# Kernel optimization log

Measured on AMD Instinct MI355X. Metric: run time of the kernel, lower is better.

## Reference

```python
import jax, jax.numpy as jnp
import numpy as np

N_HEAD = 16

def setup_inputs() -> dict:
    key = jax.random.key(0)
    ks = jax.random.split(key, 5)
    B, T, C = 2, 2048, 1024
    s = 1.0 / np.sqrt(C)
    return {
        "x":  jax.random.normal(ks[0], (B, T, C), jnp.float32),
        "Wk": jax.random.normal(ks[1], (C, C), jnp.float32) * s,
        "Wq": jax.random.normal(ks[2], (C, C), jnp.float32) * s,
        "Wv": jax.random.normal(ks[3], (C, C), jnp.float32) * s,
        "Wp": jax.random.normal(ks[4], (C, C), jnp.float32) * s,
    }

def reference(x, Wk, Wq, Wv, Wp):
    B, T, C = x.shape
    H = N_HEAD
    D = C // H
    # torch Linear (bias=False): y = x @ W.T
    def proj(W):
        return (x @ W.T).reshape(B, T, H, D).transpose(0, 2, 1, 3)  # [B,H,T,D]
    q, k, v = proj(Wq), proj(Wk), proj(Wv)
    att = jnp.einsum("bhtd,bhsd->bhts", q, k) / jnp.sqrt(jnp.float32(D))
    causal = jnp.tril(jnp.ones((T, T), dtype=bool))
    att = jnp.where(causal[None, None], att, -jnp.inf)
    att = jax.nn.softmax(att, axis=-1)
    y = jnp.einsum("bhts,bhsd->bhtd", att, v)
    y = y.transpose(0, 2, 1, 3).reshape(B, T, C)
    return y @ Wp.T
```

## Files before the change

kernel.cpp:

```cpp
#include <hip/hip_runtime.h>

typedef unsigned short u16;
typedef unsigned int u32;
typedef unsigned long long u64;
typedef __attribute__((ext_vector_type(8))) short bf16x8;
typedef __attribute__((ext_vector_type(8))) _Float16 f16x8;
typedef __attribute__((ext_vector_type(2))) _Float16 f16x2;
typedef __attribute__((ext_vector_type(4))) float f32x4;

#define GLOAD16(gp, lp) __builtin_amdgcn_global_load_lds( \
  (const __attribute__((address_space(1))) unsigned int*)(gp), \
  (__attribute__((address_space(3))) unsigned int*)(lp), 16, 0, 0)

__device__ __forceinline__ u16 f2bf(float f) {
  unsigned int u = __builtin_bit_cast(unsigned int, f);
  u += 0x7fffu + ((u >> 16) & 1u);
  return (u16)(u >> 16);
}

__device__ __forceinline__ u32 pk2(float a, float b) {
  return (u32)f2bf(a) | ((u32)f2bf(b) << 16);
}

__device__ __forceinline__ u32 pkh(float a, float b) {
  return __builtin_bit_cast(u32, __builtin_amdgcn_cvt_pkrtz(a, b));
}

__device__ __forceinline__ void wait_barrier() {
  asm volatile("s_waitcnt vmcnt(0)" ::: "memory");
  __builtin_amdgcn_s_barrier();
  __builtin_amdgcn_sched_barrier(0);
}

__global__ __launch_bounds__(256) void cvt_f32_bf16(
    const float* __restrict__ in, u16* __restrict__ out, int n) {
  int i = (blockIdx.x * 256 + threadIdx.x) * 4;
  if (i < n) {
    float4 f = *reinterpret_cast<const float4*>(in + i);
    u64 v = (u64)pk2(f.x, f.y) | ((u64)pk2(f.z, f.w) << 32);
    *reinterpret_cast<u64*>(out + i) = v;
  }
}

__global__ __launch_bounds__(256) void cvt_w4(
    const float* __restrict__ w0, const float* __restrict__ w1,
    const float* __restrict__ w2, const float* __restrict__ w3,
    u16* __restrict__ o0, u16* __restrict__ o1,
    u16* __restrict__ o2, u16* __restrict__ o3) {
  int z = blockIdx.y;
  const float* in = (z == 0) ? w0 : (z == 1) ? w1 : (z == 2) ? w2 : w3;
  u16* out = (z == 0) ? o0 : (z == 1) ? o1 : (z == 2) ? o2 : o3;
  int i = (blockIdx.x * 256 + threadIdx.x) * 4;
  float4 f = *reinterpret_cast<const float4*>(in + i);
  u64 v = (u64)pk2(f.x, f.y) | ((u64)pk2(f.z, f.w) << 32);
  *reinterpret_cast<u64*>(out + i) = v;
}

template<int MODE, int MI>
__device__ __forceinline__ void gemm_bt_body(
    const u16* __restrict__ A, const u16* __restrict__ Bw, void* __restrict__ Cout,
    int m0, int n0, float scale) {
  const int K = 1024;
  __shared__ __align__(16) u16 As[2][MI * 32 * 32];
  __shared__ __align__(16) u16 Bs[2][128 * 32];
  const int tid = threadIdx.x;
  const int lane = tid & 63, wid = tid >> 6;
  const int wr = wid >> 1, wc = wid & 1;
  const int g = lane >> 4, c = lane & 15;
  f32x4 acc[MI][4] = {};

  auto stage = [&](int buf, int k0) {
#pragma unroll
    for (int i = 0; i < MI / 2; ++i) {
      int idx = tid + i * 256;
      int row = idx >> 2, slot = idx & 3;
      int ss = slot ^ (row & 3);
      GLOAD16(A + (size_t)(m0 + row) * K + k0 + ss * 8, &As[buf][idx * 8]);
    }
#pragma unroll
    for (int i = 0; i < 2; ++i) {
      int idx = tid + i * 256;
      int row = idx >> 2, slot = idx & 3;
      int ss = slot ^ (row & 3);
      GLOAD16(Bw + (size_t)(n0 + row) * K + k0 + ss * 8, &Bs[buf][idx * 8]);
    }
  };

  stage(0, 0);
  int buf = 0;
#pragma unroll 1
  for (int kt = 0; kt < 32; ++kt) {
    wait_barrier();
    if (kt + 1 < 32) stage(buf ^ 1, (kt + 1) * 32);
    bf16x8 af[MI], bfr[4];
#pragma unroll
    for (int mi = 0; mi < MI; ++mi) {
      int row = wr * (MI * 16) + mi * 16 + c;
      int slot = g ^ (row & 3);
      af[mi] = *(const bf16x8*)&As[buf][row * 32 + slot * 8];
    }
#pragma unroll
    for (int ni = 0; ni < 4; ++ni) {
      int row = wc * 64 + ni * 16 + c;
      int slot = g ^ (row & 3);
      bfr[ni] = *(const bf16x8*)&Bs[buf][row * 32 + slot * 8];
    }
    __builtin_amdgcn_s_setprio(1);
#pragma unroll
    for (int mi = 0; mi < MI; ++mi)
#pragma unroll
      for (int ni = 0; ni < 4; ++ni)
        acc[mi][ni] = __builtin_amdgcn_mfma_f32_16x16x32_bf16(af[mi], bfr[ni], acc[mi][ni], 0, 0, 0);
    __builtin_amdgcn_s_setprio(0);
    buf ^= 1;
  }

#pragma unroll
  for (int mi = 0; mi < MI; ++mi)
#pragma unroll
    for (int ni = 0; ni < 4; ++ni)
#pragma unroll
      for (int i = 0; i < 4; ++i) {
        int m = m0 + wr * (MI * 16) + mi * 16 + g * 4 + i;
        int n = n0 + wc * 64 + ni * 16 + c;
        float v = acc[mi][ni][i];
        if (MODE == 0) {
          int b = m >> 11, t = m & 2047, h = n >> 6, d = n & 63;
          ((u16*)Cout)[(((size_t)b * 16 + h) * 2048 + t) * 64 + d] = f2bf(v * scale);
        } else {
          ((float*)Cout)[(size_t)m * 1024 + n] = v;
        }
      }
}

#define QSCALE 0.1803368801111204f

__global__ __launch_bounds__(256, 3) void proj_qkv(
    const u16* __restrict__ xb, const u16* __restrict__ wq, const u16* __restrict__ wk,
    const u16* __restrict__ wv, u16* __restrict__ q, u16* __restrict__ k, u16* __restrict__ v) {
  int z = blockIdx.z;
  const u16* W = (z == 0) ? wq : (z == 1) ? wk : wv;
  u16* O = (z == 0) ? q : (z == 1) ? k : v;
  float scale = (z == 0) ? QSCALE : 1.0f;
  gemm_bt_body<0, 4>(xb, W, O, blockIdx.y * 128, blockIdx.x * 128, scale);
}

__global__ __launch_bounds__(256, 2) void gemm_out(
    const u16* __restrict__ y, const u16* __restrict__ wp, float* __restrict__ out) {
  gemm_bt_body<1, 2>(y, wp, out, blockIdx.y * 64, blockIdx.x * 128, 1.0f);
}

__global__ __launch_bounds__(256) void transpose_v_kernel(
    const u16* __restrict__ v, u16* __restrict__ vt) {
  __shared__ u16 tile[64][65];
  int bh = blockIdx.y, t0 = blockIdx.x * 64;
  const u16* src = v + ((size_t)bh * 2048 + t0) * 64;
  u16* dst = vt + (size_t)bh * 64 * 2048 + t0;
  int tid = threadIdx.x;
#pragma unroll
  for (int i = 0; i < 16; ++i) {
    int idx = tid + i * 256;
    tile[idx >> 6][idx & 63] = src[idx];
  }
  __syncthreads();
#pragma unroll
  for (int i = 0; i < 16; ++i) {
    int idx = tid + i * 256;
    int d = idx >> 6, j = idx & 63;
    int t = ((j & 3) << 4) | (j >> 2);
    float f = __builtin_bit_cast(float, (u32)tile[t][d] << 16);
    _Float16 hh = (_Float16)f;
    dst[(size_t)d * 2048 + j] = __builtin_bit_cast(u16, hh);
  }
}

__global__ __launch_bounds__(256, 4) void attn_kernel(
    const u16* __restrict__ q, const u16* __restrict__ kg,
    const u16* __restrict__ vt, u16* __restrict__ y) {
  const int T = 2048;
  __shared__ __align__(16) u16 Ks[2][64 * 64];
  __shared__ __align__(16) u16 Vs[2][64 * 64];
  __shared__ __align__(16) u16 Ps[4][16 * 64];
  const int tid = threadIdx.x, lane = tid & 63, w = tid >> 6;
  const int g = lane >> 4, c = lane & 15;
  const int bh = blockIdx.x;
  const int qt = 31 - (int)blockIdx.y;
  const u16* Q = q + (size_t)bh * T * 64;
  const u16* K = kg + (size_t)bh * T * 64;
  const u16* V = vt + (size_t)bh * 64 * T;
  const int b = bh >> 4, h = bh & 15;
  const int qrow0 = qt * 64 + w * 16;

  f16x8 ones;
#pragma unroll
  for (int j = 0; j < 8; ++j) ones[j] = (_Float16)1.0f;

  auto stage = [&](int bb, int j0) {
#pragma unroll
    for (int i = 0; i < 2; ++i) {
      int idx = tid + i * 256;
      int row = idx >> 3, slot = idx & 7;
      int ss = slot ^ (row & 7);
      GLOAD16(K + (size_t)(j0 + row) * 64 + ss * 8, &Ks[bb][idx * 8]);
      GLOAD16(V + (size_t)row * T + j0 + ss * 8, &Vs[bb][idx * 8]);
    }
  };

  bf16x8 qf[2];
#pragma unroll
  for (int kk = 0; kk < 2; ++kk)
    qf[kk] = *(const bf16x8*)&Q[(size_t)(qrow0 + c) * 64 + kk * 32 + g * 8];

  f32x4 o[4] = {};
  f32x4 ol = {};

  const int nkt = qt + 1;
  stage(0, 0);
  int buf = 0;
#pragma unroll 1
  for (int kt = 0; kt < nkt; ++kt) {
    const int j0 = kt * 64;
    wait_barrier();
    if (kt + 1 < nkt) stage(buf ^ 1, j0 + 64);

    bf16x8 kb[4][2];
#pragma unroll
    for (int ni = 0; ni < 4; ++ni)
#pragma unroll
      for (int kk = 0; kk < 2; ++kk) {
        int kr = ni * 16 + c;
        int slot = (kk * 4 + g) ^ (kr & 7);
        kb[ni][kk] = *(const bf16x8*)&Ks[buf][kr * 64 + slot * 8];
      }
    f32x4 s[4];
    __builtin_amdgcn_s_setprio(1);
#pragma unroll
    for (int ni = 0; ni < 4; ++ni) {
      f32x4 a = {0.f, 0.f, 0.f, 0.f};
      a = __builtin_amdgcn_mfma_f32_16x16x32_bf16(qf[0], kb[ni][0], a, 0, 0, 0);
      a = __builtin_amdgcn_mfma_f32_16x16x32_bf16(qf[1], kb[ni][1], a, 0, 0, 0);
      s[ni] = a;
    }
    __builtin_amdgcn_s_setprio(0);

    const bool dumask = (kt == qt);
#pragma unroll
    for (int ni = 0; ni < 4; ++ni)
#pragma unroll
      for (int i = 0; i < 4; ++i) {
        float val = s[ni][i];
        if (dumask) {
          int row = qrow0 + g * 4 + i;
          int col = j0 + ni * 16 + c;
          if (col > row) val = -3.0e38f;
        }
        s[ni][i] = __builtin_amdgcn_exp2f(val);
      }

#pragma unroll
    for (int i = 0; i < 4; ++i) {
      int r = g * 4 + i;
      int slot = (c >> 1) ^ (r & 7);
      u64 val = (u64)pkh(s[0][i], s[1][i]) | ((u64)pkh(s[2][i], s[3][i]) << 32);
      *(u64*)((char*)&Ps[w][0] + r * 128 + slot * 16 + (c & 1) * 8) = val;
    }

    f16x8 pa[2], vb[4][2];
#pragma unroll
    for (int kk = 0; kk < 2; ++kk) {
      int slot = (kk * 4 + g) ^ (c & 7);
      pa[kk] = *(const f16x8*)&Ps[w][c * 64 + slot * 8];
    }
#pragma unroll
    for (int di = 0; di < 4; ++di)
#pragma unroll
      for (int kk = 0; kk < 2; ++kk) {
        int d = di * 16 + c;
        int slot = (kk * 4 + g) ^ (d & 7);
        vb[di][kk] = *(const f16x8*)&Vs[buf][d * 64 + slot * 8];
      }
    __builtin_amdgcn_s_setprio(1);
    ol = __builtin_amdgcn_mfma_f32_16x16x32_f16(pa[0], ones, ol, 0, 0, 0);
    ol = __builtin_amdgcn_mfma_f32_16x16x32_f16(pa[1], ones, ol, 0, 0, 0);
#pragma unroll
    for (int di = 0; di < 4; ++di) {
      o[di] = __builtin_amdgcn_mfma_f32_16x16x32_f16(pa[0], vb[di][0], o[di], 0, 0, 0);
      o[di] = __builtin_amdgcn_mfma_f32_16x16x32_f16(pa[1], vb[di][1], o[di], 0, 0, 0);
    }
    __builtin_amdgcn_s_setprio(0);
    buf ^= 1;
  }

#pragma unroll
  for (int i = 0; i < 4; ++i) {
    float inv = 1.f / ol[i];
    int t = qrow0 + g * 4 + i;
#pragma unroll
    for (int di = 0; di < 4; ++di) {
      int col = h * 64 + di * 16 + c;
      y[((size_t)b * 2048 + t) * 1024 + col] = f2bf(o[di][i] * inv);
    }
  }
}

extern "C" void kernel_launch(void* const* d_in, const int* in_sizes, int n_in,
                              void* d_out, int out_size, void* d_ws, size_t ws_size,
                              hipStream_t stream) {
  const float* x  = (const float*)d_in[0];
  const float* Wk = (const float*)d_in[1];
  const float* Wq = (const float*)d_in[2];
  const float* Wv = (const float*)d_in[3];
  const float* Wp = (const float*)d_in[4];
  float* out = (float*)d_out;

  char* ws = (char*)d_ws;
  const size_t SZ_X = (size_t)4096 * 1024 * 2;
  const size_t SZ_W = (size_t)1024 * 1024 * 2;
  u16* xb  = (u16*)(ws);
  u16* qb  = (u16*)(ws + SZ_X);
  u16* kb  = (u16*)(ws + 2 * SZ_X);
  u16* vb  = (u16*)(ws + 3 * SZ_X);
  u16* wqb = (u16*)(ws + 4 * SZ_X);
  u16* wkb = (u16*)(ws + 4 * SZ_X + SZ_W);
  u16* wvb = (u16*)(ws + 4 * SZ_X + 2 * SZ_W);
  u16* wpb = (u16*)(ws + 4 * SZ_X + 3 * SZ_W);

  cvt_f32_bf16<<<4096, 256, 0, stream>>>(x, xb, 4096 * 1024);
  cvt_w4<<<dim3(1024, 4), 256, 0, stream>>>(Wq, Wk, Wv, Wp, wqb, wkb, wvb, wpb);

  proj_qkv<<<dim3(8, 32, 3), 256, 0, stream>>>(xb, wqb, wkb, wvb, qb, kb, vb);

  u16* vtb = xb;
  transpose_v_kernel<<<dim3(32, 32), 256, 0, stream>>>(vb, vtb);

  u16* yb = vb;
  attn_kernel<<<dim3(32, 32), 256, 0, stream>>>(qb, kb, vtb, yb);

  gemm_out<<<dim3(8, 64), 256, 0, stream>>>(yb, wpb, out);
}
```

Baseline: 114.4 us.

## Shrink attention tiles to 32x32 with two-wave blocks for finer causal granularity

Attention blocks now cover 32 query rows with 2 waves (128 threads) and step over 32-key tiles instead of 64/64 with 4 waves. The V transpose permutation, LDS staging, swizzles and P layout change to match the 32-wide key chunks. The aim is more blocks, less wasted work on the causal diagonal and better load balance. In exchange each K/V tile is reused by fewer query rows, so global and LDS traffic per FLOP and the number of barriers per unit of work go up.

```diff
diff --git a/kernel.cpp b/kernel.cpp
--- a/kernel.cpp
+++ b/kernel.cpp
@@ -5,7 +5,6 @@
 typedef unsigned long long u64;
 typedef __attribute__((ext_vector_type(8))) short bf16x8;
 typedef __attribute__((ext_vector_type(8))) _Float16 f16x8;
-typedef __attribute__((ext_vector_type(2))) _Float16 f16x2;
 typedef __attribute__((ext_vector_type(4))) float f32x4;
 
 #define GLOAD16(gp, lp) __builtin_amdgcn_global_load_lds( \
@@ -166,30 +165,31 @@
 #pragma unroll
   for (int i = 0; i < 16; ++i) {
     int idx = tid + i * 256;
-    int d = idx >> 6, j = idx & 63;
-    int t = ((j & 3) << 4) | (j >> 2);
+    int d = idx >> 6, jj = idx & 63;
+    int sub = jj >> 5, j5 = jj & 31;
+    int t = sub * 32 + ((j5 & 1) << 4) + (j5 >> 1);
     float f = __builtin_bit_cast(float, (u32)tile[t][d] << 16);
     _Float16 hh = (_Float16)f;
-    dst[(size_t)d * 2048 + j] = __builtin_bit_cast(u16, hh);
-  }
-}
-
-__global__ __launch_bounds__(256, 4) void attn_kernel(
+    dst[(size_t)d * 2048 + jj] = __builtin_bit_cast(u16, hh);
+  }
+}
+
+__global__ __launch_bounds__(128, 4) void attn_kernel(
     const u16* __restrict__ q, const u16* __restrict__ kg,
     const u16* __restrict__ vt, u16* __restrict__ y) {
   const int T = 2048;
-  __shared__ __align__(16) u16 Ks[2][64 * 64];
-  __shared__ __align__(16) u16 Vs[2][64 * 64];
-  __shared__ __align__(16) u16 Ps[4][16 * 64];
+  __shared__ __align__(16) u16 Ks[2][32 * 64];
+  __shared__ __align__(16) u16 Vs[2][64 * 32];
+  __shared__ __align__(16) u16 Ps[2][16 * 32];
   const int tid = threadIdx.x, lane = tid & 63, w = tid >> 6;
   const int g = lane >> 4, c = lane & 15;
   const int bh = blockIdx.x;
-  const int qt = 31 - (int)blockIdx.y;
+  const int qt = 63 - (int)blockIdx.y;
   const u16* Q = q + (size_t)bh * T * 64;
   const u16* K = kg + (size_t)bh * T * 64;
   const u16* V = vt + (size_t)bh * 64 * T;
   const int b = bh >> 4, h = bh & 15;
-  const int qrow0 = qt * 64 + w * 16;
+  const int qrow0 = qt * 32 + w * 16;
 
   f16x8 ones;
 #pragma unroll
@@ -198,11 +198,17 @@
   auto stage = [&](int bb, int j0) {
 #pragma unroll
     for (int i = 0; i < 2; ++i) {
-      int idx = tid + i * 256;
+      int idx = tid + i * 128;
       int row = idx >> 3, slot = idx & 7;
       int ss = slot ^ (row & 7);
       GLOAD16(K + (size_t)(j0 + row) * 64 + ss * 8, &Ks[bb][idx * 8]);
-      GLOAD16(V + (size_t)row * T + j0 + ss * 8, &Vs[bb][idx * 8]);
+    }
+#pragma unroll
+    for (int i = 0; i < 2; ++i) {
+      int idx = tid + i * 128;
+      int d = idx >> 2, ch = idx & 3;
+      int ss = ch ^ (d & 3);
+      GLOAD16(V + (size_t)d * T + j0 + ss * 8, &Vs[bb][idx * 8]);
     }
   };
 
@@ -219,23 +225,23 @@
   int buf = 0;
 #pragma unroll 1
   for (int kt = 0; kt < nkt; ++kt) {
-    const int j0 = kt * 64;
+    const int j0 = kt * 32;
     wait_barrier();
-    if (kt + 1 < nkt) stage(buf ^ 1, j0 + 64);
-
-    bf16x8 kb[4][2];
-#pragma unroll
-    for (int ni = 0; ni < 4; ++ni)
+    if (kt + 1 < nkt) stage(buf ^ 1, j0 + 32);
+
+    bf16x8 kb[2][2];
+#pragma unroll
+    for (int ni = 0; ni < 2; ++ni)
 #pragma unroll
       for (int kk = 0; kk < 2; ++kk) {
         int kr = ni * 16 + c;
         int slot = (kk * 4 + g) ^ (kr & 7);
         kb[ni][kk] = *(const bf16x8*)&Ks[buf][kr * 64 + slot * 8];
       }
-    f32x4 s[4];
+    f32x4 s[2];
     __builtin_amdgcn_s_setprio(1);
 #pragma unroll
-    for (int ni = 0; ni < 4; ++ni) {
+    for (int ni = 0; ni < 2; ++ni) {
       f32x4 a = {0.f, 0.f, 0.f, 0.f};
       a = __builtin_amdgcn_mfma_f32_16x16x32_bf16(qf[0], kb[ni][0], a, 0, 0, 0);
       a = __builtin_amdgcn_mfma_f32_16x16x32_bf16(qf[1], kb[ni][1], a, 0, 0, 0);
@@ -245,7 +251,7 @@
 
     const bool dumask = (kt == qt);
 #pragma unroll
-    for (int ni = 0; ni < 4; ++ni)
+    for (int ni = 0; ni < 2; ++ni)
 #pragma unroll
       for (int i = 0; i < 4; ++i) {
         float val = s[ni][i];
@@ -260,33 +266,22 @@
 #pragma unroll
     for (int i = 0; i < 4; ++i) {
       int r = g * 4 + i;
-      int slot = (c >> 1) ^ (r & 7);
-      u64 val = (u64)pkh(s[0][i], s[1][i]) | ((u64)pkh(s[2][i], s[3][i]) << 32);
-      *(u64*)((char*)&Ps[w][0] + r * 128 + slot * 16 + (c & 1) * 8) = val;
-    }
-
-    f16x8 pa[2], vb[4][2];
-#pragma unroll
-    for (int kk = 0; kk < 2; ++kk) {
-      int slot = (kk * 4 + g) ^ (c & 7);
-      pa[kk] = *(const f16x8*)&Ps[w][c * 64 + slot * 8];
-    }
+      int byteoff = r * 64 + (((c >> 2) ^ (r & 3)) << 4) + ((c & 3) << 2);
+      *(u32*)((char*)&Ps[w][0] + byteoff) = pkh(s[0][i], s[1][i]);
+    }
+
+    f16x8 pa = *(const f16x8*)((char*)&Ps[w][0] + c * 64 + ((g ^ (c & 3)) << 4));
+    f16x8 vb[4];
+#pragma unroll
+    for (int di = 0; di < 4; ++di) {
+      int d = di * 16 + c;
+      vb[di] = *(const f16x8*)((char*)&Vs[buf][0] + d * 64 + ((g ^ (d & 3)) << 4));
+    }
+    __builtin_amdgcn_s_setprio(1);
+    ol = __builtin_amdgcn_mfma_f32_16x16x32_f16(pa, ones, ol, 0, 0, 0);
 #pragma unroll
     for (int di = 0; di < 4; ++di)
-#pragma unroll
-      for (int kk = 0; kk < 2; ++kk) {
-        int d = di * 16 + c;
-        int slot = (kk * 4 + g) ^ (d & 7);
-        vb[di][kk] = *(const f16x8*)&Vs[buf][d * 64 + slot * 8];
-      }
-    __builtin_amdgcn_s_setprio(1);
-    ol = __builtin_amdgcn_mfma_f32_16x16x32_f16(pa[0], ones, ol, 0, 0, 0);
-    ol = __builtin_amdgcn_mfma_f32_16x16x32_f16(pa[1], ones, ol, 0, 0, 0);
-#pragma unroll
-    for (int di = 0; di < 4; ++di) {
-      o[di] = __builtin_amdgcn_mfma_f32_16x16x32_f16(pa[0], vb[di][0], o[di], 0, 0, 0);
-      o[di] = __builtin_amdgcn_mfma_f32_16x16x32_f16(pa[1], vb[di][1], o[di], 0, 0, 0);
-    }
+      o[di] = __builtin_amdgcn_mfma_f32_16x16x32_f16(pa, vb[di], o[di], 0, 0, 0);
     __builtin_amdgcn_s_setprio(0);
     buf ^= 1;
   }
@@ -334,7 +329,7 @@
   transpose_v_kernel<<<dim3(32, 32), 256, 0, stream>>>(vb, vtb);
 
   u16* yb = vb;
-  attn_kernel<<<dim3(32, 32), 256, 0, stream>>>(qb, kb, vtb, yb);
+  attn_kernel<<<dim3(32, 64), 128, 0, stream>>>(qb, kb, vtb, yb);
 
   gemm_out<<<dim3(8, 64), 256, 0, stream>>>(yb, wpb, out);
 }
```

New measurement: 126.0 us. 1.1x slower.
